# Performance work log

Measured on AMD Instinct MI355X. Metric: run time of the kernel, lower is better.

Reference implementation:

```python
import jax, jax.numpy as jnp
import numpy as np

CUTOFF = 5.0
RBF_DIM = 32
M0, M1, M2 = 128, 64, 32          # node multiplicities for l=0,1,2
DIM_NODE = M0 + 3 * M1 + 5 * M2   # 480
MSG = 64                          # message multiplicity per l
NBLK = 3
MAX_Z = 100


def _sph_harm(d):
    # component-normalized real spherical harmonics up to lmax=2; d: [E,3] unit vectors
    x, y, z = d[:, 0], d[:, 1], d[:, 2]
    s3, s5, s15 = jnp.sqrt(3.0), jnp.sqrt(5.0), jnp.sqrt(15.0)
    return jnp.stack([
        jnp.ones_like(x),
        s3 * x, s3 * y, s3 * z,
        s15 * x * y, s15 * y * z, 0.5 * s5 * (3.0 * z * z - 1.0),
        s15 * x * z, 0.5 * s15 * (x * x - y * y),
    ], axis=-1)  # [E, 9]


def _rbf(d):
    centers = jnp.linspace(0.0, CUTOFF, RBF_DIM)
    width = CUTOFF / (RBF_DIM - 1)
    return jnp.exp(-0.5 * ((d[:, None] - centers) / width) ** 2)  # [E, RBF_DIM]


def _irrep_norm(x):
    # per-node RMS norm of each irrep block (l=0,1,2)
    eps = 1e-6
    parts = []
    for off, mul, dim in ((0, M0, 1), (M0, M1, 3), (M0 + 3 * M1, M2, 5)):
        blk = x[:, off:off + mul * dim].reshape(-1, mul, dim)
        rms = jnp.sqrt(jnp.mean(jnp.sum(blk * blk, axis=-1), axis=-1, keepdims=True) + eps)
        parts.append((blk / rms[..., None]).reshape(-1, mul * dim))
    return jnp.concatenate(parts, axis=-1)


def setup_inputs() -> dict:
    key = jax.random.key(0)
    ks = jax.random.split(key, 20)
    B, N, E = 32, 128, 131072
    BN = B * N

    z = jax.random.randint(ks[0], (B, N), 1, MAX_Z + 1)
    mask = jnp.ones((B, N), jnp.float32)
    edge_src = jax.random.randint(ks[1], (E,), 0, BN)
    edge_dst = jax.random.randint(ks[2], (E,), 0, BN)
    edge_weight = jax.random.uniform(ks[3], (E,), minval=0.1, maxval=CUTOFF)
    ed = jax.random.normal(ks[4], (E, 3), jnp.float32)
    ed = ed / jnp.linalg.norm(ed, axis=-1, keepdims=True)
    edge_vec = ed * edge_weight[:, None]

    def nrm(k, shape, fan_in):
        return jax.random.normal(k, shape, jnp.float32) / np.sqrt(fan_in)

    params = {
        "z_emb": jax.random.normal(ks[5], (MAX_Z + 1, M0), jnp.float32),
        "W_in": nrm(ks[6], (M0, M0), M0),
        "Wp": nrm(ks[7], (NBLK, M0, 3 * MSG), M0),
        "rW1": nrm(ks[8], (NBLK, RBF_DIM, 64), RBF_DIM),
        "rb1": jnp.zeros((NBLK, 64), jnp.float32),
        "rW2": nrm(ks[9], (NBLK, 64, 3 * MSG), 64),
        "rb2": jnp.zeros((NBLK, 3 * MSG), jnp.float32),
        "Wo0": nrm(ks[10], (NBLK, MSG, M0), MSG),
        "Wo1": nrm(ks[11], (NBLK, MSG, M1), MSG),
        "Wo2": nrm(ks[12], (NBLK, MSG, M2), MSG),
        "res_scale": jnp.full((NBLK,), 1.0, jnp.float32),
    }
    return {"z": z, "mask": mask, "edge_src": edge_src, "edge_dst": edge_dst,
            "edge_weight": edge_weight, "edge_vec": edge_vec, **params}


def reference(z, mask, edge_src, edge_dst, edge_weight, edge_vec,
              z_emb, W_in, Wp, rW1, rb1, rW2, rb2, Wo0, Wo1, Wo2, res_scale):
    B, N = z.shape
    BN = B * N
    fmask = mask.reshape(BN)

    # element embedding -> o3.Linear(0e -> irreps_node): only scalar channels are produced
    zf = z_emb[z.reshape(BN)]                                    # [BN, node_attr]
    x0 = zf @ W_in                                               # [BN, M0]
    x = jnp.concatenate([x0, jnp.zeros((BN, DIM_NODE - M0), x0.dtype)], axis=-1)
    x = x * fmask[:, None]

    elen = edge_weight
    edir = edge_vec / jnp.clip(elen, 1e-8)[:, None]
    rbf = _rbf(jnp.minimum(elen, CUTOFF))                        # [E, RBF_DIM]
    sh = _sph_harm(edir)                                         # [E, 9]
    fcut = 0.5 * (jnp.cos(jnp.pi * jnp.minimum(elen / CUTOFF, 1.0)) + 1.0)

    for b in range(NBLK):
        s = x[:, :M0]
        proj = s[edge_src] @ Wp[b]                               # [E, 3*MSG] gather + GEMM
        h = jax.nn.silu(rbf @ rW1[b] + rb1[b])
        r = h @ rW2[b] + rb2[b]                                  # [E, 3*MSG] radial weights
        w = proj * r * fcut[:, None]
        w0, w1, w2 = w[:, :MSG], w[:, MSG:2 * MSG], w[:, 2 * MSG:]
        msg0 = w0 * sh[:, 0:1]                                   # [E, MSG]
        msg1 = w1[:, :, None] * sh[:, None, 1:4]                 # [E, MSG, 3]
        msg2 = w2[:, :, None] * sh[:, None, 4:9]                 # [E, MSG, 5]
        m0 = jax.ops.segment_sum(msg0, edge_dst, num_segments=BN)
        m1 = jax.ops.segment_sum(msg1, edge_dst, num_segments=BN)
        m2 = jax.ops.segment_sum(msg2, edge_dst, num_segments=BN)
        u0 = m0 @ Wo0[b]                                         # [BN, M0]
        u1 = jnp.einsum('ncd,ck->nkd', m1, Wo1[b]).reshape(BN, 3 * M1)
        u2 = jnp.einsum('ncd,ck->nkd', m2, Wo2[b]).reshape(BN, 5 * M2)
        x = x + res_scale[b] * jnp.concatenate([u0, u1, u2], axis=-1)

    x = _irrep_norm(x) * fmask[:, None]
    return x.reshape(B, N, DIM_NODE)
```

## Files before the change

kernel.cpp:

```cpp
#include <hip/hip_runtime.h>
#include <math.h>

#define M0 128
#define M1 64
#define M2 32
#define DIMN 480
#define MSGC 64
#define NBLK 3
#define RBFD 32
#define NT 512
#define TCHUNK 32
#define NNP 16
#define GNPB 4
#define PSTR 68
#define WROWS 224
#define FCUT 5.0f

typedef unsigned int   u32;
typedef unsigned short u16;

__device__ __forceinline__ u16 f2bf(float f) {
    u32 u = __float_as_uint(f);
    u32 r = (u + 0x7fffu + ((u >> 16) & 1u)) >> 16;
    return (u16)r;
}
__device__ __forceinline__ float bf_lo(u32 v) { return __uint_as_float(v << 16); }
__device__ __forceinline__ float bf_hi(u32 v) { return __uint_as_float(v & 0xffff0000u); }

struct __align__(16) ERec {
    int   src;
    int   ti;
    float fr;
    float fc;
    float sh[8];
};

__global__ void k_zero(int* __restrict__ p, int n) {
    int i = blockIdx.x * blockDim.x + threadIdx.x;
    if (i < n) p[i] = 0;
}

__global__ void k_count(const int* __restrict__ dst, int* __restrict__ counts, int E) {
    int e = blockIdx.x * blockDim.x + threadIdx.x;
    if (e >= E) return;
    atomicAdd(&counts[dst[e]], 1);
}

__global__ __launch_bounds__(1024) void k_scan(const int* __restrict__ counts,
                                               int* __restrict__ offs,
                                               int* __restrict__ cursor, int n) {
    __shared__ int ws[1024];
    int t = threadIdx.x;
    int4 v = ((const int4*)counts)[t];
    int s0 = v.x, s1 = s0 + v.y, s2 = s1 + v.z, s3 = s2 + v.w;
    ws[t] = s3;
    __syncthreads();
    for (int d = 1; d < 1024; d <<= 1) {
        int val = (t >= d) ? ws[t - d] : 0;
        __syncthreads();
        ws[t] += val;
        __syncthreads();
    }
    int excl = (t == 0) ? 0 : ws[t - 1];
    int4 o;
    o.x = excl; o.y = excl + s0; o.z = excl + s1; o.w = excl + s2;
    ((int4*)offs)[t] = o;
    ((int4*)cursor)[t] = o;
    if (t == 1023) offs[n] = excl + s3;
}

__global__ void k_build(const float* __restrict__ ew, const float* __restrict__ ev,
                        const int* __restrict__ src, const int* __restrict__ dst,
                        int* __restrict__ cursor, ERec* __restrict__ rec, int E) {
    int e = blockIdx.x * blockDim.x + threadIdx.x;
    if (e >= E) return;
    float len = ew[e];
    float inv = 1.0f / fmaxf(len, 1e-8f);
    float x = ev[e * 3 + 0] * inv;
    float y = ev[e * 3 + 1] * inv;
    float z = ev[e * 3 + 2] * inv;
    const float s3 = 1.7320508075688772f, s5 = 2.23606797749979f, s15 = 3.872983346207417f;
    ERec r;
    r.src = src[e];
    float u = fminf(len, FCUT) * ((float)(NT - 1) / FCUT);
    int ti = (int)u;
    ti = min(ti, NT - 2);
    r.ti = ti;
    r.fr = u - (float)ti;
    float t = fminf(len / FCUT, 1.0f);
    r.fc = 0.5f * (cosf(3.14159265358979323846f * t) + 1.0f);
    r.sh[0] = s3 * x;
    r.sh[1] = s3 * y;
    r.sh[2] = s3 * z;
    r.sh[3] = s15 * x * y;
    r.sh[4] = s15 * y * z;
    r.sh[5] = 0.5f * s5 * (3.0f * z * z - 1.0f);
    r.sh[6] = s15 * x * z;
    r.sh[7] = 0.5f * s15 * (x * x - y * y);
    int p = atomicAdd(&cursor[dst[e]], 1);
    rec[p] = r;
}

__global__ __launch_bounds__(128) void k_initx(const int* __restrict__ z,
                                               const float* __restrict__ mask,
                                               const float* __restrict__ zemb,
                                               const float* __restrict__ Win,
                                               float* __restrict__ x) {
    int n = blockIdx.x;
    __shared__ float zf[M0];
    int zi = z[n];
    for (int k = threadIdx.x; k < M0; k += blockDim.x) zf[k] = zemb[zi * M0 + k];
    __syncthreads();
    int j = threadIdx.x;
    float acc = 0.0f;
    for (int k = 0; k < M0; ++k) acc += zf[k] * Win[k * M0 + j];
    float fm = mask[n];
    x[(size_t)n * DIMN + j] = acc * fm;
    for (int t = M0 + j; t < DIMN; t += M0) x[(size_t)n * DIMN + t] = 0.0f;
}

__global__ __launch_bounds__(256) void k_rtab(const float* __restrict__ rW1,
                                              const float* __restrict__ rb1,
                                              const float* __restrict__ rW2,
                                              const float* __restrict__ rb2,
                                              float* __restrict__ rS) {
    int blk = blockIdx.x;
    int b = blk / (NT / TCHUNK);
    int t0 = (blk % (NT / TCHUNK)) * TCHUNK;
    int tid = threadIdx.x;
    __shared__ float rbf_s[TCHUNK][RBFD];
    __shared__ float hh_s[64][TCHUNK];

    const float wdt = FCUT / (float)(RBFD - 1);
    for (int idx = tid; idx < TCHUNK * RBFD; idx += 256) {
        int tt = idx >> 5, k = idx & 31;
        float len = (float)(t0 + tt) * (FCUT / (float)(NT - 1));
        float d0 = (len - (float)k * wdt) / wdt;
        rbf_s[tt][k] = expf(-0.5f * d0 * d0);
    }
    __syncthreads();
    const float* W1 = rW1 + b * RBFD * 64;
    for (int idx = tid; idx < TCHUNK * 64; idx += 256) {
        int tt = idx >> 6, jj = idx & 63;
        float a = rb1[b * 64 + jj];
        #pragma unroll 8
        for (int k = 0; k < RBFD; ++k) a += rbf_s[tt][k] * W1[k * 64 + jj];
        hh_s[jj][tt] = a / (1.0f + expf(-a));
    }
    __syncthreads();
    if (tid < 192) {
        int c = tid;
        const float* W2 = rW2 + b * 64 * 192;
        float b2 = rb2[b * 192 + c];
        float* out = rS + (size_t)b * NT * 192;
        for (int g = 0; g < TCHUNK / 8; ++g) {
            float acc[8];
            #pragma unroll
            for (int u = 0; u < 8; ++u) acc[u] = b2;
            for (int k = 0; k < 64; ++k) {
                float w2 = W2[k * 192 + c];
                const float4* hp = (const float4*)&hh_s[k][g * 8];
                float4 h0 = hp[0], h1 = hp[1];
                acc[0] += h0.x * w2; acc[1] += h0.y * w2;
                acc[2] += h0.z * w2; acc[3] += h0.w * w2;
                acc[4] += h1.x * w2; acc[5] += h1.y * w2;
                acc[6] += h1.z * w2; acc[7] += h1.w * w2;
            }
            #pragma unroll
            for (int u = 0; u < 8; ++u) {
                int t = t0 + g * 8 + u;
                out[(size_t)t * 192 + c] = acc[u];
            }
        }
    }
}

__global__ void k_prep(const float* __restrict__ rS, u32* __restrict__ rPI,
                       const float* __restrict__ Wo0, const float* __restrict__ Wo1,
                       const float* __restrict__ Wo2, float* __restrict__ WoT) {
    int idx = blockIdx.x * blockDim.x + threadIdx.x;
    const int totalP = NBLK * NT * 192;
    if (idx < totalP) {
        int c = idx % 192;
        int t = (idx / 192) % NT;
        int b = idx / (192 * NT);
        float lo = rS[idx];
        float hi = (t < NT - 1) ? rS[idx + 192] : lo;
        int lane = c & 63, q = c >> 6;
        rPI[(((size_t)b * NT + t) * 64 + lane) * 4 + q] =
            (u32)f2bf(lo) | ((u32)f2bf(hi) << 16);
        return;
    }
    int w = idx - totalP;
    const int wtot = NBLK * WROWS * 64;
    if (w >= wtot) return;
    int b = w / (WROWS * 64);
    int rem = w - b * (WROWS * 64);
    int row = rem >> 6, c = rem & 63;
    float v;
    if (row < 128)      v = Wo0[(size_t)b * MSGC * M0 + c * M0 + row];
    else if (row < 192) v = Wo1[(size_t)b * MSGC * M1 + c * M1 + (row - 128)];
    else                v = Wo2[(size_t)b * MSGC * M2 + c * M2 + (row - 192)];
    WoT[w] = v;
}

__global__ __launch_bounds__(192) void k_proj(const float* __restrict__ x,
                                              const float* __restrict__ Wp,
                                              u16* __restrict__ PI) {
    int n0 = blockIdx.x * NNP;
    int j = threadIdx.x;
    __shared__ float xs[NNP][M0];
    for (int idx = j; idx < NNP * M0; idx += 192) {
        int n = idx >> 7, c = idx & 127;
        xs[n][c] = x[(size_t)(n0 + n) * DIMN + c];
    }
    __syncthreads();
    float acc[NNP];
    #pragma unroll
    for (int u = 0; u < NNP; ++u) acc[u] = 0.0f;
    for (int k = 0; k < M0; ++k) {
        float wv = Wp[k * 192 + j];
        #pragma unroll
        for (int u = 0; u < NNP; ++u) acc[u] += xs[u][k] * wv;
    }
    int lane = j & 63, q = j >> 6;
    #pragma unroll
    for (int u = 0; u < NNP; ++u)
        PI[((size_t)(n0 + u) * 64 + lane) * 4 + q] = f2bf(acc[u]);
}

__global__ __launch_bounds__(512) void k_gather(const u16* __restrict__ PI,
                                                const u32* __restrict__ rPI,
                                                const ERec* __restrict__ rec,
                                                const int* __restrict__ offs,
                                                const float* __restrict__ WoT,
                                                const float* __restrict__ res_scale, int b,
                                                float* __restrict__ x,
                                                const float* __restrict__ mask,
                                                float* __restrict__ out) {
    int t = threadIdx.x;
    int w = t >> 6;
    int j = t & 63;
    int local = w >> 1;
    int par = w & 1;
    int n0 = blockIdx.x * GNPB;
    int n = n0 + local;
    int e0 = offs[n], e1 = offs[n + 1];

    float m0 = 0.0f;
    float m1a[3] = {0, 0, 0};
    float m2a[5] = {0, 0, 0, 0, 0};

    __shared__ float mbuf[8][9 * PSTR];
    __shared__ float invs[GNPB][3];

    {
        int i = e0 + par;
        if (i < e1) {
            const int last = e1 - 1;
            float4 A0, A1, A2, B0, B1, B2, C0, C1, C2;
            {
                int ia = __builtin_amdgcn_readfirstlane(i);
                const float4* p = (const float4*)(rec + ia);
                A0 = p[0]; A1 = p[1]; A2 = p[2];
            }
            {
                int v = i + 2; v = v < e1 ? v : last;
                int ib = __builtin_amdgcn_readfirstlane(v);
                const float4* p = (const float4*)(rec + ib);
                B0 = p[0]; B1 = p[1]; B2 = p[2];
            }
            {
                int v = i + 4; v = v < e1 ? v : last;
                int ic = __builtin_amdgcn_readfirstlane(v);
                const float4* p = (const float4*)(rec + ic);
                C0 = p[0]; C1 = p[1]; C2 = p[2];
            }
            uint4 rA, rB, rC; uint2 pA, pB, pC;
            {
                int s = __float_as_int(A0.x), ti = __float_as_int(A0.y);
                rA = ((const uint4*)(rPI + ((size_t)ti << 8)))[j];
                pA = ((const uint2*)(PI + ((size_t)s << 8)))[j];
            }
            {
                int s = __float_as_int(B0.x), ti = __float_as_int(B0.y);
                rB = ((const uint4*)(rPI + ((size_t)ti << 8)))[j];
                pB = ((const uint2*)(PI + ((size_t)s << 8)))[j];
            }
            for (; i < e1; i += 2) {
                float4 D0, D1, D2;
                {
                    int v = i + 6; v = v < e1 ? v : last;
                    int id = __builtin_amdgcn_readfirstlane(v);
                    const float4* p = (const float4*)(rec + id);
                    D0 = p[0]; D1 = p[1]; D2 = p[2];
                }
                {
                    int s = __float_as_int(C0.x), ti = __float_as_int(C0.y);
                    rC = ((const uint4*)(rPI + ((size_t)ti << 8)))[j];
                    pC = ((const uint2*)(PI + ((size_t)s << 8)))[j];
                }
                float fr = A0.z, fc = A0.w;
                float la = bf_lo(rA.x);
                float va = la + fr * (bf_hi(rA.x) - la);
                float p0 = __uint_as_float(pA.x << 16);
                float p1 = __uint_as_float(pA.x & 0xffff0000u);
                float p2 = __uint_as_float(pA.y << 16);
                m0 = fmaf(p0 * va, fc, m0);
                float lb = bf_lo(rA.y);
                float vb = lb + fr * (bf_hi(rA.y) - lb);
                float w1 = p1 * vb * fc;
                m1a[0] += w1 * A1.x;
                m1a[1] += w1 * A1.y;
                m1a[2] += w1 * A1.z;
                float lc = bf_lo(rA.z);
                float vc = lc + fr * (bf_hi(rA.z) - lc);
                float w2 = p2 * vc * fc;
                m2a[0] += w2 * A1.w;
                m2a[1] += w2 * A2.x;
                m2a[2] += w2 * A2.y;
                m2a[3] += w2 * A2.z;
                m2a[4] += w2 * A2.w;
                A0 = B0; A1 = B1; A2 = B2;
                B0 = C0; B1 = C1; B2 = C2;
                C0 = D0; C1 = D1; C2 = D2;
                rA = rB; pA = pB; rB = rC; pB = pC;
            }
        }
    }

    mbuf[w][0 * PSTR + j] = m0;
    #pragma unroll
    for (int d = 0; d < 3; ++d) mbuf[w][(1 + d) * PSTR + j] = m1a[d];
    #pragma unroll
    for (int d = 0; d < 5; ++d) mbuf[w][(4 + d) * PSTR + j] = m2a[d];
    __syncthreads();
    #pragma unroll
    for (int u = 0; u < GNPB; ++u)
        for (int c = t; c < 9 * PSTR; c += 512)
            mbuf[2 * u][c] += mbuf[2 * u + 1][c];
    __syncthreads();

    float rs = res_scale[b];
    int o = t;
    if (o < DIMN) {
        int row, mbase;
        if (o < M0) {
            row = o; mbase = 0;
        } else if (o < M0 + 3 * M1) {
            int q = o - M0, k = q / 3, d = q - 3 * k;
            row = 128 + k; mbase = (1 + d) * PSTR;
        } else {
            int q = o - (M0 + 3 * M1), k = q / 5, d = q - 5 * k;
            row = 192 + k; mbase = (4 + d) * PSTR;
        }
        const float4* Wv = (const float4*)(WoT + (size_t)row * 64);
        float a0 = 0, a1 = 0, a2 = 0, a3 = 0;
        #pragma unroll
        for (int c4 = 0; c4 < 16; ++c4) {
            float4 wv = Wv[c4];
            float4 v0 = *(const float4*)&mbuf[0][mbase + 4 * c4];
            float4 v1 = *(const float4*)&mbuf[2][mbase + 4 * c4];
            float4 v2 = *(const float4*)&mbuf[4][mbase + 4 * c4];
            float4 v3 = *(const float4*)&mbuf[6][mbase + 4 * c4];
            a0 += wv.x * v0.x + wv.y * v0.y + wv.z * v0.z + wv.w * v0.w;
            a1 += wv.x * v1.x + wv.y * v1.y + wv.z * v1.z + wv.w * v1.w;
            a2 += wv.x * v2.x + wv.y * v2.y + wv.z * v2.z + wv.w * v2.w;
            a3 += wv.x * v3.x + wv.y * v3.y + wv.z * v3.z + wv.w * v3.w;
        }
        if (b < NBLK - 1) {
            x[(size_t)(n0 + 0) * DIMN + o] += rs * a0;
            x[(size_t)(n0 + 1) * DIMN + o] += rs * a1;
            x[(size_t)(n0 + 2) * DIMN + o] += rs * a2;
            x[(size_t)(n0 + 3) * DIMN + o] += rs * a3;
        } else {
            mbuf[1][o] = x[(size_t)(n0 + 0) * DIMN + o] + rs * a0;
            mbuf[3][o] = x[(size_t)(n0 + 1) * DIMN + o] + rs * a1;
            mbuf[5][o] = x[(size_t)(n0 + 2) * DIMN + o] + rs * a2;
            mbuf[7][o] = x[(size_t)(n0 + 3) * DIMN + o] + rs * a3;
        }
    }

    if (b < NBLK - 1) return;

    __syncthreads();
    if (w < GNPB) {
        const float* xf = mbuf[2 * w + 1];
        float s0 = 0, s1 = 0, s2 = 0;
        for (int c = j; c < DIMN; c += 64) {
            float v = xf[c];
            if (c < 128) s0 += v * v;
            else if (c < 320) s1 += v * v;
            else s2 += v * v;
        }
        #pragma unroll
        for (int d = 32; d > 0; d >>= 1) {
            s0 += __shfl_down(s0, d);
            s1 += __shfl_down(s1, d);
            s2 += __shfl_down(s2, d);
        }
        if (j == 0) {
            invs[w][0] = rsqrtf(s0 / (float)M0 + 1e-6f);
            invs[w][1] = rsqrtf(s1 / (float)M1 + 1e-6f);
            invs[w][2] = rsqrtf(s2 / (float)M2 + 1e-6f);
        }
    }
    __syncthreads();
    if (o < DIMN) {
        int cls = (o < 128) ? 0 : (o < 320) ? 1 : 2;
        #pragma unroll
        for (int u = 0; u < GNPB; ++u) {
            float fm = mask[n0 + u];
            out[(size_t)(n0 + u) * DIMN + o] = mbuf[2 * u + 1][o] * invs[u][cls] * fm;
        }
    }
}

extern "C" void kernel_launch(void* const* d_in, const int* in_sizes, int n_in,
                              void* d_out, int out_size, void* d_ws, size_t ws_size,
                              hipStream_t stream) {
    const int*   z    = (const int*)d_in[0];
    const float* mask = (const float*)d_in[1];
    const int*   esrc = (const int*)d_in[2];
    const int*   edst = (const int*)d_in[3];
    const float* ew   = (const float*)d_in[4];
    const float* ev   = (const float*)d_in[5];
    const float* zemb = (const float*)d_in[6];
    const float* Win  = (const float*)d_in[7];
    const float* Wp   = (const float*)d_in[8];
    const float* rW1  = (const float*)d_in[9];
    const float* rb1  = (const float*)d_in[10];
    const float* rW2  = (const float*)d_in[11];
    const float* rb2  = (const float*)d_in[12];
    const float* Wo0  = (const float*)d_in[13];
    const float* Wo1  = (const float*)d_in[14];
    const float* Wo2  = (const float*)d_in[15];
    const float* res  = (const float*)d_in[16];

    const int BN = in_sizes[0];
    const int E  = in_sizes[2];

    char* w = (char*)d_ws;
    float* x    = (float*)w;  w += (size_t)BN * DIMN * 4;
    u16*   PI   = (u16*)w;    w += (size_t)BN * 256 * 2;
    float* rS   = (float*)w;  w += (size_t)NBLK * NT * 192 * 4;
    u32*   rPI  = (u32*)w;    w += (size_t)NBLK * NT * 256 * 4;
    ERec*  rec  = (ERec*)w;   w += (size_t)E * sizeof(ERec);
    float* WoT  = (float*)w;  w += (size_t)NBLK * WROWS * 64 * 4;
    int* counts = (int*)w;   w += (size_t)BN * 4;
    int* offs   = (int*)w;   w += (size_t)(BN + 4) * 4;
    int* cursor = (int*)w;   w += (size_t)BN * 4;

    k_zero<<<(BN + 255) / 256, 256, 0, stream>>>(counts, BN);
    k_count<<<(E + 255) / 256, 256, 0, stream>>>(edst, counts, E);
    k_scan<<<1, 1024, 0, stream>>>(counts, offs, cursor, BN);
    k_build<<<(E + 255) / 256, 256, 0, stream>>>(ew, ev, esrc, edst, cursor, rec, E);
    k_initx<<<BN, 128, 0, stream>>>(z, mask, zemb, Win, x);
    k_rtab<<<NBLK * (NT / TCHUNK), 256, 0, stream>>>(rW1, rb1, rW2, rb2, rS);
    {
        int total = NBLK * NT * 192 + NBLK * WROWS * 64;
        k_prep<<<(total + 255) / 256, 256, 0, stream>>>(rS, rPI, Wo0, Wo1, Wo2, WoT);
    }

    for (int b = 0; b < NBLK; ++b) {
        k_proj<<<BN / NNP, 192, 0, stream>>>(x, Wp + (size_t)b * M0 * 192, PI);
        k_gather<<<BN / GNPB, 512, 0, stream>>>(PI, rPI + (size_t)b * NT * 256, rec, offs,
                                                WoT + (size_t)b * WROWS * 64,
                                                res, b, x, mask, (float*)d_out);
    }
}
```

Measured before the change: 226.3 us.

## Fuse radial table packing, init and first projection; fold cutoff into SH

The radial table kernel now writes the packed bf16 lo/hi interpolation pairs directly, which removes the intermediate fp32 table and the separate prep kernel. The Wo transpose rides along as extra blocks of the same launch. Node init is fused with the block-0 projection into one kernel. The cosine cutoff is pre-multiplied into the stored spherical harmonics, so the gather drops two multiplies per edge, and its edge loop is rewritten with a fixed trip count and unroll. This saves launches and memory passes but adds redundant boundary row computation per chunk and higher register use in the table kernel.

```diff
diff --git a/kernel.cpp b/kernel.cpp
--- a/kernel.cpp
+++ b/kernel.cpp
@@ -88,60 +88,63 @@
     r.ti = ti;
     r.fr = u - (float)ti;
     float t = fminf(len / FCUT, 1.0f);
-    r.fc = 0.5f * (cosf(3.14159265358979323846f * t) + 1.0f);
-    r.sh[0] = s3 * x;
-    r.sh[1] = s3 * y;
-    r.sh[2] = s3 * z;
-    r.sh[3] = s15 * x * y;
-    r.sh[4] = s15 * y * z;
-    r.sh[5] = 0.5f * s5 * (3.0f * z * z - 1.0f);
-    r.sh[6] = s15 * x * z;
-    r.sh[7] = 0.5f * s15 * (x * x - y * y);
+    float fc = 0.5f * (cosf(3.14159265358979323846f * t) + 1.0f);
+    r.fc = fc;
+    r.sh[0] = s3 * x * fc;
+    r.sh[1] = s3 * y * fc;
+    r.sh[2] = s3 * z * fc;
+    r.sh[3] = s15 * x * y * fc;
+    r.sh[4] = s15 * y * z * fc;
+    r.sh[5] = 0.5f * s5 * (3.0f * z * z - 1.0f) * fc;
+    r.sh[6] = s15 * x * z * fc;
+    r.sh[7] = 0.5f * s15 * (x * x - y * y) * fc;
     int p = atomicAdd(&cursor[dst[e]], 1);
     rec[p] = r;
 }
 
-__global__ __launch_bounds__(128) void k_initx(const int* __restrict__ z,
-                                               const float* __restrict__ mask,
-                                               const float* __restrict__ zemb,
-                                               const float* __restrict__ Win,
-                                               float* __restrict__ x) {
-    int n = blockIdx.x;
-    __shared__ float zf[M0];
-    int zi = z[n];
-    for (int k = threadIdx.x; k < M0; k += blockDim.x) zf[k] = zemb[zi * M0 + k];
-    __syncthreads();
-    int j = threadIdx.x;
-    float acc = 0.0f;
-    for (int k = 0; k < M0; ++k) acc += zf[k] * Win[k * M0 + j];
-    float fm = mask[n];
-    x[(size_t)n * DIMN + j] = acc * fm;
-    for (int t = M0 + j; t < DIMN; t += M0) x[(size_t)n * DIMN + t] = 0.0f;
-}
-
+#define RTB (NBLK * (NT / TCHUNK))
 __global__ __launch_bounds__(256) void k_rtab(const float* __restrict__ rW1,
                                               const float* __restrict__ rb1,
                                               const float* __restrict__ rW2,
                                               const float* __restrict__ rb2,
-                                              float* __restrict__ rS) {
+                                              u32* __restrict__ rPI,
+                                              const float* __restrict__ Wo0,
+                                              const float* __restrict__ Wo1,
+                                              const float* __restrict__ Wo2,
+                                              float* __restrict__ WoT) {
     int blk = blockIdx.x;
+    int tid = threadIdx.x;
+    if (blk >= RTB) {
+        int idx = (blk - RTB) * 256 + tid;
+        const int wtot = NBLK * WROWS * 64;
+        if (idx >= wtot) return;
+        int b = idx / (WROWS * 64);
+        int rem = idx - b * (WROWS * 64);
+        int row = rem >> 6, c = rem & 63;
+        float v;
+        if (row < 128)      v = Wo0[(size_t)b * MSGC * M0 + c * M0 + row];
+        else if (row < 192) v = Wo1[(size_t)b * MSGC * M1 + c * M1 + (row - 128)];
+        else                v = Wo2[(size_t)b * MSGC * M2 + c * M2 + (row - 192)];
+        WoT[idx] = v;
+        return;
+    }
     int b = blk / (NT / TCHUNK);
     int t0 = (blk % (NT / TCHUNK)) * TCHUNK;
-    int tid = threadIdx.x;
-    __shared__ float rbf_s[TCHUNK][RBFD];
-    __shared__ float hh_s[64][TCHUNK];
+    __shared__ float rbf_s[TCHUNK + 1][RBFD];
+    __shared__ float hh_s[64][TCHUNK + 1];
 
     const float wdt = FCUT / (float)(RBFD - 1);
-    for (int idx = tid; idx < TCHUNK * RBFD; idx += 256) {
+    for (int idx = tid; idx < (TCHUNK + 1) * RBFD; idx += 256) {
         int tt = idx >> 5, k = idx & 31;
-        float len = (float)(t0 + tt) * (FCUT / (float)(NT - 1));
+        int te = min(t0 + tt, NT - 1);
+        float len = (float)te * (FCUT / (float)(NT - 1));
         float d0 = (len - (float)k * wdt) / wdt;
         rbf_s[tt][k] = expf(-0.5f * d0 * d0);
     }
     __syncthreads();
     const float* W1 = rW1 + b * RBFD * 64;
-    for (int idx = tid; idx < TCHUNK * 64; idx += 256) {
-        int tt = idx >> 6, jj = idx & 63;
+    for (int idx = tid; idx < (TCHUNK + 1) * 64; idx += 256) {
+        int tt = idx / 64, jj = idx & 63;
         float a = rb1[b * 64 + jj];
         #pragma unroll 8
         for (int k = 0; k < RBFD; ++k) a += rbf_s[tt][k] * W1[k * 64 + jj];
@@ -151,57 +154,68 @@
     if (tid < 192) {
         int c = tid;
         const float* W2 = rW2 + b * 64 * 192;
+        float w2r[64];
+        #pragma unroll
+        for (int k = 0; k < 64; ++k) w2r[k] = W2[k * 192 + c];
         float b2 = rb2[b * 192 + c];
-        float* out = rS + (size_t)b * NT * 192;
-        for (int g = 0; g < TCHUNK / 8; ++g) {
-            float acc[8];
+        int lane = c & 63, q = c >> 6;
+        u32* out = rPI + ((size_t)b * NT * 64) * 4;
+        float prev = 0.0f;
+        for (int tt = 0; tt <= TCHUNK; ++tt) {
+            float acc = b2;
             #pragma unroll
-            for (int u = 0; u < 8; ++u) acc[u] = b2;
-            for (int k = 0; k < 64; ++k) {
-                float w2 = W2[k * 192 + c];
-                const float4* hp = (const float4*)&hh_s[k][g * 8];
-                float4 h0 = hp[0], h1 = hp[1];
-                acc[0] += h0.x * w2; acc[1] += h0.y * w2;
-                acc[2] += h0.z * w2; acc[3] += h0.w * w2;
-                acc[4] += h1.x * w2; acc[5] += h1.y * w2;
-                acc[6] += h1.z * w2; acc[7] += h1.w * w2;
-            }
-            #pragma unroll
-            for (int u = 0; u < 8; ++u) {
-                int t = t0 + g * 8 + u;
-                out[(size_t)t * 192 + c] = acc[u];
-            }
-        }
-    }
-}
-
-__global__ void k_prep(const float* __restrict__ rS, u32* __restrict__ rPI,
-                       const float* __restrict__ Wo0, const float* __restrict__ Wo1,
-                       const float* __restrict__ Wo2, float* __restrict__ WoT) {
-    int idx = blockIdx.x * blockDim.x + threadIdx.x;
-    const int totalP = NBLK * NT * 192;
-    if (idx < totalP) {
-        int c = idx % 192;
-        int t = (idx / 192) % NT;
-        int b = idx / (192 * NT);
-        float lo = rS[idx];
-        float hi = (t < NT - 1) ? rS[idx + 192] : lo;
-        int lane = c & 63, q = c >> 6;
-        rPI[(((size_t)b * NT + t) * 64 + lane) * 4 + q] =
-            (u32)f2bf(lo) | ((u32)f2bf(hi) << 16);
-        return;
-    }
-    int w = idx - totalP;
-    const int wtot = NBLK * WROWS * 64;
-    if (w >= wtot) return;
-    int b = w / (WROWS * 64);
-    int rem = w - b * (WROWS * 64);
-    int row = rem >> 6, c = rem & 63;
-    float v;
-    if (row < 128)      v = Wo0[(size_t)b * MSGC * M0 + c * M0 + row];
-    else if (row < 192) v = Wo1[(size_t)b * MSGC * M1 + c * M1 + (row - 128)];
-    else                v = Wo2[(size_t)b * MSGC * M2 + c * M2 + (row - 192)];
-    WoT[w] = v;
+            for (int k = 0; k < 64; ++k) acc += hh_s[k][tt] * w2r[k];
+            if (tt > 0) {
+                int t = t0 + tt - 1;
+                out[((size_t)t * 64 + lane) * 4 + q] =
+                    (u32)f2bf(prev) | ((u32)f2bf(acc) << 16);
+            }
+            prev = acc;
+        }
+    }
+}
+
+__global__ __launch_bounds__(192) void k_proj0(const int* __restrict__ z,
+                                               const float* __restrict__ mask,
+                                               const float* __restrict__ zemb,
+                                               const float* __restrict__ Win,
+                                               const float* __restrict__ Wp,
+                                               float* __restrict__ x,
+                                               u16* __restrict__ PI) {
+    int n0 = blockIdx.x * NNP;
+    int j = threadIdx.x;
+    __shared__ float zf[NNP][M0];
+    __shared__ float xs[NNP][M0];
+    for (int idx = j; idx < NNP * M0; idx += 192) {
+        int n = idx >> 7, c = idx & 127;
+        zf[n][c] = zemb[z[n0 + n] * M0 + c];
+    }
+    __syncthreads();
+    for (int idx = j; idx < NNP * M0; idx += 192) {
+        int n = idx >> 7, c = idx & 127;
+        float acc = 0.0f;
+        for (int k = 0; k < M0; ++k) acc += zf[n][k] * Win[k * M0 + c];
+        acc *= mask[n0 + n];
+        xs[n][c] = acc;
+        x[(size_t)(n0 + n) * DIMN + c] = acc;
+    }
+    for (int idx = j; idx < NNP * (DIMN - M0); idx += 192) {
+        int n = idx / (DIMN - M0), c = idx - n * (DIMN - M0);
+        x[(size_t)(n0 + n) * DIMN + M0 + c] = 0.0f;
+    }
+    __syncthreads();
+    float acc[NNP];
+    #pragma unroll
+    for (int u = 0; u < NNP; ++u) acc[u] = 0.0f;
+    for (int k = 0; k < M0; ++k) {
+        float wv = Wp[k * 192 + j];
+        #pragma unroll
+        for (int u = 0; u < NNP; ++u) acc[u] += xs[u][k] * wv;
+    }
+    int lane = j & 63, q = j >> 6;
+    #pragma unroll
+    for (int u = 0; u < NNP; ++u)
+        PI[((size_t)(n0 + u) * 64 + lane) * 4 + q] = f2bf(acc[u]);
 }
 
 __global__ __launch_bounds__(192) void k_proj(const float* __restrict__ x,
@@ -255,23 +269,24 @@
     __shared__ float invs[GNPB][3];
 
     {
-        int i = e0 + par;
-        if (i < e1) {
+        int i0 = e0 + par;
+        if (i0 < e1) {
             const int last = e1 - 1;
+            int nIter = (e1 - i0 + 1) >> 1;
             float4 A0, A1, A2, B0, B1, B2, C0, C1, C2;
             {
-                int ia = __builtin_amdgcn_readfirstlane(i);
+                int ia = __builtin_amdgcn_readfirstlane(i0);
                 const float4* p = (const float4*)(rec + ia);
                 A0 = p[0]; A1 = p[1]; A2 = p[2];
             }
             {
-                int v = i + 2; v = v < e1 ? v : last;
+                int v = i0 + 2; v = v < e1 ? v : last;
                 int ib = __builtin_amdgcn_readfirstlane(v);
                 const float4* p = (const float4*)(rec + ib);
                 B0 = p[0]; B1 = p[1]; B2 = p[2];
             }
             {
-                int v = i + 4; v = v < e1 ? v : last;
+                int v = i0 + 4; v = v < e1 ? v : last;
                 int ic = __builtin_amdgcn_readfirstlane(v);
                 const float4* p = (const float4*)(rec + ic);
                 C0 = p[0]; C1 = p[1]; C2 = p[2];
@@ -287,7 +302,9 @@
                 rB = ((const uint4*)(rPI + ((size_t)ti << 8)))[j];
                 pB = ((const uint2*)(PI + ((size_t)s << 8)))[j];
             }
-            for (; i < e1; i += 2) {
+            #pragma unroll 4
+            for (int k = 0; k < nIter; ++k) {
+                int i = i0 + (k << 1);
                 float4 D0, D1, D2;
                 {
                     int v = i + 6; v = v < e1 ? v : last;
@@ -309,13 +326,13 @@
                 m0 = fmaf(p0 * va, fc, m0);
                 float lb = bf_lo(rA.y);
                 float vb = lb + fr * (bf_hi(rA.y) - lb);
-                float w1 = p1 * vb * fc;
+                float w1 = p1 * vb;
                 m1a[0] += w1 * A1.x;
                 m1a[1] += w1 * A1.y;
                 m1a[2] += w1 * A1.z;
                 float lc = bf_lo(rA.z);
                 float vc = lc + fr * (bf_hi(rA.z) - lc);
-                float w2 = p2 * vc * fc;
+                float w2 = p2 * vc;
                 m2a[0] += w2 * A1.w;
                 m2a[1] += w2 * A2.x;
                 m2a[2] += w2 * A2.y;
@@ -443,7 +460,6 @@
     char* w = (char*)d_ws;
     float* x    = (float*)w;  w += (size_t)BN * DIMN * 4;
     u16*   PI   = (u16*)w;    w += (size_t)BN * 256 * 2;
-    float* rS   = (float*)w;  w += (size_t)NBLK * NT * 192 * 4;
     u32*   rPI  = (u32*)w;    w += (size_t)NBLK * NT * 256 * 4;
     ERec*  rec  = (ERec*)w;   w += (size_t)E * sizeof(ERec);
     float* WoT  = (float*)w;  w += (size_t)NBLK * WROWS * 64 * 4;
@@ -455,15 +471,16 @@
     k_count<<<(E + 255) / 256, 256, 0, stream>>>(edst, counts, E);
     k_scan<<<1, 1024, 0, stream>>>(counts, offs, cursor, BN);
     k_build<<<(E + 255) / 256, 256, 0, stream>>>(ew, ev, esrc, edst, cursor, rec, E);
-    k_initx<<<BN, 128, 0, stream>>>(z, mask, zemb, Win, x);
-    k_rtab<<<NBLK * (NT / TCHUNK), 256, 0, stream>>>(rW1, rb1, rW2, rb2, rS);
     {
-        int total = NBLK * NT * 192 + NBLK * WROWS * 64;
-        k_prep<<<(total + 255) / 256, 256, 0, stream>>>(rS, rPI, Wo0, Wo1, Wo2, WoT);
-    }
+        int wotb = (NBLK * WROWS * 64 + 255) / 256;
+        k_rtab<<<RTB + wotb, 256, 0, stream>>>(rW1, rb1, rW2, rb2, rPI,
+                                               Wo0, Wo1, Wo2, WoT);
+    }
+    k_proj0<<<BN / NNP, 192, 0, stream>>>(z, mask, zemb, Win, Wp, x, PI);
 
     for (int b = 0; b < NBLK; ++b) {
-        k_proj<<<BN / NNP, 192, 0, stream>>>(x, Wp + (size_t)b * M0 * 192, PI);
+        if (b > 0)
+            k_proj<<<BN / NNP, 192, 0, stream>>>(x, Wp + (size_t)b * M0 * 192, PI);
         k_gather<<<BN / GNPB, 512, 0, stream>>>(PI, rPI + (size_t)b * NT * 256, rec, offs,
                                                 WoT + (size_t)b * WROWS * 64,
                                                 res, b, x, mask, (float*)d_out);
```

Result: faster. 216.9 us (-4.2%).
